# Performance work log

Measured on AMD Instinct MI355X. Metric: run time of the kernel, lower is better.

## Reference

```python
import jax, jax.numpy as jnp
import numpy as np

N_HEAD = 16
LN_EPS = 1e-5


def _layernorm(x, g, b):
    mu = jnp.mean(x, axis=-1, keepdims=True)
    var = jnp.mean(jnp.square(x - mu), axis=-1, keepdims=True)
    return (x - mu) * jax.lax.rsqrt(var + LN_EPS) * g + b


def setup_inputs() -> dict:
    key = jax.random.key(0)
    ks = jax.random.split(key, 12)
    B, S, D = 2, 2048, 1024
    F = 4 * D
    std = 0.02
    return {
        "x": jax.random.normal(ks[0], (B, S, D), jnp.float32),
        "w_attn": jax.random.normal(ks[1], (D, 3 * D), jnp.float32) * std,
        "b_attn": jnp.zeros((3 * D,), jnp.float32),
        "w_o": jax.random.normal(ks[2], (D, D), jnp.float32) * std,
        "b_o": jnp.zeros((D,), jnp.float32),
        "ln1_g": jnp.ones((D,), jnp.float32),
        "ln1_b": jnp.zeros((D,), jnp.float32),
        "w_fc": jax.random.normal(ks[3], (D, F), jnp.float32) * std,
        "b_fc": jnp.zeros((F,), jnp.float32),
        "w_pr": jax.random.normal(ks[4], (F, D), jnp.float32) * std,
        "b_pr": jnp.zeros((D,), jnp.float32),
        "ln2_g": jnp.ones((D,), jnp.float32),
        "ln2_b": jnp.zeros((D,), jnp.float32),
    }


def reference(x, w_attn, b_attn, w_o, b_o, ln1_g, ln1_b,
              w_fc, b_fc, w_pr, b_pr, ln2_g, ln2_b):
    B, S, D = x.shape
    H = N_HEAD
    hd = D // H

    # --- attention ---
    qkv = x @ w_attn + b_attn                      # [B,S,3D]
    q, k, v = jnp.split(qkv, 3, axis=-1)
    q = q.reshape(B, S, H, hd).transpose(0, 2, 1, 3)  # [B,H,S,hd]
    k = k.reshape(B, S, H, hd).transpose(0, 2, 1, 3)
    v = v.reshape(B, S, H, hd).transpose(0, 2, 1, 3)

    # scores in fp32, scaled by sqrt(head_dim) (scale=True)
    w = jnp.einsum('bhqd,bhkd->bhqk', q.astype(jnp.float32),
                   k.astype(jnp.float32)) / jnp.sqrt(jnp.float32(hd))
    bias = jnp.tril(jnp.ones((S, S), jnp.float32))     # causal mask slice of registered buffer
    w = w * bias + (-10000.0) * (1.0 - bias)
    a = jax.nn.softmax(w, axis=-1).astype(v.dtype)
    o = jnp.einsum('bhqk,bhkd->bhqd', a, v)            # [B,H,S,hd]
    o = o.transpose(0, 2, 1, 3).reshape(B, S, D)
    a_out = o @ w_o + b_o

    # --- post-LN residual + MLP (gelu, d_ff = 4D) ---
    n = _layernorm(x + a_out, ln1_g, ln1_b)
    m = jax.nn.gelu(n @ w_fc + b_fc, approximate=False) @ w_pr + b_pr
    h = _layernorm(n + m, ln2_g, ln2_b)
    return h
```

## Files before the change

### kernel.cpp

```cpp
#include <hip/hip_runtime.h>
#include <stdint.h>
#include <math.h>


typedef __attribute__((ext_vector_type(4))) float f32x4;
typedef __attribute__((ext_vector_type(8))) short s16x8;

__device__ __forceinline__ float bf2f(short s){
  unsigned u = ((unsigned)(unsigned short)s) << 16;
  return __builtin_bit_cast(float, u);
}
__device__ __forceinline__ short f2bf(float f){
  unsigned u = __builtin_bit_cast(unsigned, f);
  unsigned r = (u + 0x7fffu + ((u >> 16) & 1u)) >> 16;
  return (short)(unsigned short)r;
}

__device__ __forceinline__ void gload_lds16(const void* gp, void* lp){
  __builtin_amdgcn_global_load_lds(
      (__attribute__((address_space(1))) void*)const_cast<void*>(gp),
      (__attribute__((address_space(3))) void*)lp,
      16, 0, 0);
}

__global__ void cvt_f32_bf16(const float* __restrict__ in, short* __restrict__ out, int n){
  int i = (blockIdx.x * blockDim.x + threadIdx.x) * 4;
  if (i < n){
    float4 v = *(const float4*)(in + i);
    short4 o;
    o.x = f2bf(v.x); o.y = f2bf(v.y); o.z = f2bf(v.z); o.w = f2bf(v.w);
    *(short4*)(out + i) = o;
  }
}

__global__ __launch_bounds__(256) void wtrans(const float* __restrict__ in,
                                              short* __restrict__ out, int R, int C){
  __shared__ float tile[32][33];
  int c0 = blockIdx.x * 32, r0 = blockIdx.y * 32;
  int tx = threadIdx.x, ty = threadIdx.y;
  #pragma unroll
  for (int j = 0; j < 4; ++j)
    tile[ty + j*8][tx] = in[(size_t)(r0 + ty + j*8) * C + c0 + tx];
  __syncthreads();
  #pragma unroll
  for (int j = 0; j < 4; ++j)
    out[(size_t)(c0 + ty + j*8) * R + r0 + tx] = f2bf(tile[tx][ty + j*8]);
}

__global__ __launch_bounds__(256) void vtrans(const short* __restrict__ qkv,
                                              short* __restrict__ vt){
  __shared__ short tile[32][33];
  int bh = blockIdx.z; int b = bh >> 4, h = bh & 15;
  int s0 = blockIdx.x * 32, d0 = blockIdx.y * 32;
  int tx = threadIdx.x, ty = threadIdx.y;
  #pragma unroll
  for (int j = 0; j < 4; ++j)
    tile[ty + j*8][tx] = qkv[(size_t)(b*2048 + s0 + ty + j*8) * 3072 + 2048 + h*64 + d0 + tx];
  __syncthreads();
  #pragma unroll
  for (int j = 0; j < 4; ++j)
    vt[(size_t)(bh*64 + d0 + ty + j*8) * 2048 + s0 + tx] = tile[tx][ty + j*8];
}

#define TBK 32

__global__ __launch_bounds__(512, 2) void gemm256(
    const short* __restrict__ A, const short* __restrict__ BT,
    const float* __restrict__ bias,
    void* __restrict__ o0, void* __restrict__ o1,
    void* __restrict__ o2, void* __restrict__ o3,
    int M, int N, int K, int EPI, int KS)
{
  __shared__ __attribute__((aligned(16))) short lds[4][16384];
  const int t = threadIdx.x;
  const int lane = t & 63;
  const int wid = t >> 6;
  const int wr = wid >> 2, wc = wid & 3;
  const int lrow = lane & 15, lk = lane >> 4;

  const int gx = gridDim.x;
  const int nwg = gx * gridDim.y;
  const int P = blockIdx.y * gx + blockIdx.x;
  const int wg = (P & 7) * (nwg >> 3) + (P >> 3);
  const int m0 = (wg / gx) * 256, n0 = (wg % gx) * 256;

  const int Kspl = K / KS;
  const int kbeg = blockIdx.z * Kspl;
  const int NT = Kspl / TBK;

  const short* srcA[2]; const short* srcB[2]; int ldso[2];
  #pragma unroll
  for (int q = 0; q < 2; ++q){
    int o = q*8192 + t*16;
    int row = o >> 6;
    int chunk = ((o >> 4) & 3) ^ ((row >> 1) & 3);
    ldso[q] = o;
    srcA[q] = A  + (size_t)(m0 + row) * K + kbeg + chunk * 8;
    srcB[q] = BT + (size_t)(n0 + row) * K + kbeg + chunk * 8;
  }

  int aoff[8], boff[4];
  #pragma unroll
  for (int m = 0; m < 8; ++m){
    int row = wr*128 + m*16 + lrow;
    aoff[m] = row*32 + (lk ^ ((row >> 1) & 3))*8;
  }
  #pragma unroll
  for (int n = 0; n < 4; ++n){
    int row = wc*64 + n*16 + lrow;
    boff[n] = 8192 + row*32 + (lk ^ ((row >> 1) & 3))*8;
  }

  auto stage = [&](int tile){
    const int s = tile & 3;
    const int ko = tile * TBK;
    #pragma unroll
    for (int q = 0; q < 2; ++q){
      gload_lds16(srcA[q] + ko, (char*)&lds[s][0] + ldso[q]);
      gload_lds16(srcB[q] + ko, (char*)&lds[s][0] + 16384 + ldso[q]);
    }
  };

  f32x4 acc[8][4] = {};

  stage(0);
  stage(1);
  for (int tt = 0; tt < NT; ++tt){
    if (tt < NT - 1) asm volatile("s_waitcnt vmcnt(4)" ::: "memory");
    else             asm volatile("s_waitcnt vmcnt(0)" ::: "memory");
    __builtin_amdgcn_s_barrier();
    __builtin_amdgcn_sched_barrier(0);

    if (tt + 2 < NT) stage(tt + 2);

    const short* lp = &lds[tt & 3][0];
    s16x8 afr[8], bfr[4];
    #pragma unroll
    for (int n = 0; n < 4; ++n) bfr[n] = *(const s16x8*)(lp + boff[n]);
    #pragma unroll
    for (int m = 0; m < 8; ++m) afr[m] = *(const s16x8*)(lp + aoff[m]);

    asm volatile("s_waitcnt lgkmcnt(0)" ::: "memory");
    __builtin_amdgcn_sched_barrier(0);
    __builtin_amdgcn_s_setprio(1);
    #pragma unroll
    for (int m = 0; m < 8; ++m)
      #pragma unroll
      for (int n = 0; n < 4; ++n)
        acc[m][n] = __builtin_amdgcn_mfma_f32_16x16x32_bf16(afr[m], bfr[n], acc[m][n], 0, 0, 0);
    __builtin_amdgcn_s_setprio(0);
  }

  void* pz = (blockIdx.z == 0) ? o0 : (blockIdx.z == 1) ? o1
           : (blockIdx.z == 2) ? o2 : o3;
  #pragma unroll
  for (int m = 0; m < 8; ++m){
    #pragma unroll
    for (int n = 0; n < 4; ++n){
      #pragma unroll
      for (int r = 0; r < 4; ++r){
        int row = m0 + wr*128 + m*16 + lk*4 + r;
        int col = n0 + wc*64  + n*16 + lrow;
        size_t idx = (size_t)row * N + col;
        if (EPI == 4){
          ((short*)pz)[idx] = f2bf(acc[m][n][r]);
        } else {
          float v = acc[m][n][r] + bias[col];
          if (EPI == 0){
            ((short*)o0)[idx] = f2bf(v);
          } else {
            float g = 0.5f * v * (1.0f + erff(v * 0.70710678118654752f));
            ((short*)o0)[idx] = f2bf(g);
          }
        }
      }
    }
  }
}

__global__ __launch_bounds__(256, 2) void attn_kernel(
    const short* __restrict__ qkv, const short* __restrict__ vt,
    short* __restrict__ ob)
{
  const int P = blockIdx.x;
  const int xcd = P & 7;
  const int idx = P >> 3;
  const int pairi = idx & 15;
  const int bh = xcd + ((idx >> 4) << 3);
  const int b = bh >> 4, h = bh & 15;
  const int t  = threadIdx.x;
  const int lane = t & 63;
  const int w = t >> 6;
  const int lrow = lane & 15, lk = lane >> 4;

  __shared__ short sK[2][64*64];
  __shared__ short sV[2][64*64];
  __shared__ short sP[4][16][68];

  const size_t kgbase = (size_t)(b*2048)*3072 + 1024 + h*64;
  const size_t vgbase = (size_t)((b*16 + h)*64)*2048;

  auto stage = [&](int buf, int k0){
    #pragma unroll
    for (int r2 = 0; r2 < 2; ++r2){
      int o = r2*4096 + t*16;
      int row = o >> 7;
      int lsl = ((o >> 4) & 7) ^ (row & 7);
      gload_lds16(qkv + kgbase + (size_t)(k0 + row)*3072 + lsl*8, (char*)sK[buf] + o);
      gload_lds16(vt  + vgbase + (size_t)row*2048 + k0   + lsl*8, (char*)sV[buf] + o);
    }
  };

  for (int pass = 0; pass < 2; ++pass){
    const int qt = pass ? 31 - pairi : pairi;
    const int q0 = qt * 64;
    const int qbase = q0 + w * 16;

    s16x8 aq[2];
    #pragma unroll
    for (int kc = 0; kc < 2; ++kc)
      aq[kc] = *(const s16x8*)(qkv + (size_t)(b*2048 + qbase + lrow)*3072 + h*64 + kc*32 + lk*8);

    f32x4 oacc[4] = {};
    float mrun[4], lrun[4];
    #pragma unroll
    for (int r = 0; r < 4; ++r){ mrun[r] = -1e30f; lrun[r] = 0.0f; }

    const int nt = qt + 1;
    __syncthreads();
    stage(0, 0);
    __syncthreads();
    int cur = 0;

    for (int ktile = 0; ktile < nt; ++ktile){
      const int k0 = ktile * 64;
      if (ktile + 1 < nt) stage(cur ^ 1, k0 + 64);

      f32x4 sacc[4] = {};
      __builtin_amdgcn_s_setprio(1);
      #pragma unroll
      for (int kc = 0; kc < 2; ++kc){
        #pragma unroll
        for (int ct = 0; ct < 4; ++ct){
          int row = ct*16 + lrow;
          int slot = (kc*4 + lk) ^ (row & 7);
          s16x8 bk = *(const s16x8*)&sK[cur][row*64 + slot*8];
          sacc[ct] = __builtin_amdgcn_mfma_f32_16x16x32_bf16(aq[kc], bk, sacc[ct], 0, 0, 0);
        }
      }
      __builtin_amdgcn_s_setprio(0);

      float s[4][4];
      const bool need_mask = (k0 + 63 > qbase);
      #pragma unroll
      for (int ct = 0; ct < 4; ++ct){
        #pragma unroll
        for (int r = 0; r < 4; ++r){
          float v = sacc[ct][r] * 0.125f;
          if (need_mask){
            int qi = qbase + lk*4 + r;
            int ki = k0 + ct*16 + lrow;
            if (ki > qi) v = -10000.0f;
          }
          s[ct][r] = v;
        }
      }

      #pragma unroll
      for (int r = 0; r < 4; ++r){
        float mx = fmaxf(fmaxf(s[0][r], s[1][r]), fmaxf(s[2][r], s[3][r]));
        #pragma unroll
        for (int off = 1; off < 16; off <<= 1)
          mx = fmaxf(mx, __shfl_xor(mx, off, 64));
        float mnew = fmaxf(mrun[r], mx);
        float sf = __expf(mrun[r] - mnew);
        lrun[r] *= sf;
        #pragma unroll
        for (int dt = 0; dt < 4; ++dt) oacc[dt][r] *= sf;
        float ts = 0.0f;
        #pragma unroll
        for (int ct = 0; ct < 4; ++ct){
          float p = __expf(s[ct][r] - mnew);
          s[ct][r] = p;
          ts += p;
        }
        #pragma unroll
        for (int off = 1; off < 16; off <<= 1)
          ts += __shfl_xor(ts, off, 64);
        lrun[r] += ts;
        mrun[r] = mnew;
      }

      #pragma unroll
      for (int ct = 0; ct < 4; ++ct)
        #pragma unroll
        for (int r = 0; r < 4; ++r)
          sP[w][lk*4 + r][ct*16 + lrow] = f2bf(s[ct][r]);

      s16x8 pa[2];
      #pragma unroll
      for (int kc = 0; kc < 2; ++kc)
        pa[kc] = *(const s16x8*)&sP[w][lrow][kc*32 + lk*8];
      __builtin_amdgcn_s_setprio(1);
      #pragma unroll
      for (int dt = 0; dt < 4; ++dt){
        #pragma unroll
        for (int kc = 0; kc < 2; ++kc){
          int row = dt*16 + lrow;
          int slot = (kc*4 + lk) ^ (row & 7);
          s16x8 bv = *(const s16x8*)&sV[cur][row*64 + slot*8];
          oacc[dt] = __builtin_amdgcn_mfma_f32_16x16x32_bf16(pa[kc], bv, oacc[dt], 0, 0, 0);
        }
      }
      __builtin_amdgcn_s_setprio(0);

      __syncthreads();
      cur ^= 1;
    }

    #pragma unroll
    for (int r = 0; r < 4; ++r){
      float inv = 1.0f / lrun[r];
      int row = b*2048 + qbase + lk*4 + r;
      #pragma unroll
      for (int dt = 0; dt < 4; ++dt){
        int col = h*64 + dt*16 + lrow;
        ob[(size_t)row * 1024 + col] = f2bf(oacc[dt][r] * inv);
      }
    }
  }
}

__global__ __launch_bounds__(256) void ln_fused(
    const short* __restrict__ p0, const short* __restrict__ p1,
    const short* __restrict__ p2, const short* __restrict__ p3,
    const float* __restrict__ bias,
    const short* __restrict__ resid_bf, const float* __restrict__ resid_f,
    const float* __restrict__ g, const float* __restrict__ b,
    void* __restrict__ out, int bf16_out)
{
  const int row = blockIdx.x;
  const int t = threadIdx.x;
  const size_t base = (size_t)row*1024 + t*4;
  short4 a0 = *(const short4*)(p0 + base);
  short4 a1 = *(const short4*)(p1 + base);
  short4 a2 = *(const short4*)(p2 + base);
  short4 a3 = *(const short4*)(p3 + base);
  float4 bi = *(const float4*)(bias + t*4);
  float r0, r1, r2, r3;
  if (resid_bf){
    short4 rr = *(const short4*)(resid_bf + base);
    r0 = bf2f(rr.x); r1 = bf2f(rr.y); r2 = bf2f(rr.z); r3 = bf2f(rr.w);
  } else {
    float4 rr = *(const float4*)(resid_f + base);
    r0 = rr.x; r1 = rr.y; r2 = rr.z; r3 = rr.w;
  }
  float v0 = bf2f(a0.x) + bf2f(a1.x) + bf2f(a2.x) + bf2f(a3.x) + bi.x + r0;
  float v1 = bf2f(a0.y) + bf2f(a1.y) + bf2f(a2.y) + bf2f(a3.y) + bi.y + r1;
  float v2 = bf2f(a0.z) + bf2f(a1.z) + bf2f(a2.z) + bf2f(a3.z) + bi.z + r2;
  float v3 = bf2f(a0.w) + bf2f(a1.w) + bf2f(a2.w) + bf2f(a3.w) + bi.w + r3;
  float s = v0 + v1 + v2 + v3;
  float q = v0*v0 + v1*v1 + v2*v2 + v3*v3;
  #pragma unroll
  for (int off = 1; off < 64; off <<= 1){
    s += __shfl_xor(s, off, 64);
    q += __shfl_xor(q, off, 64);
  }
  __shared__ float ss[4], sq[4];
  if ((t & 63) == 0){ ss[t >> 6] = s; sq[t >> 6] = q; }
  __syncthreads();
  s = ss[0] + ss[1] + ss[2] + ss[3];
  q = sq[0] + sq[1] + sq[2] + sq[3];
  float mu = s * (1.0f/1024.0f);
  float var = q * (1.0f/1024.0f) - mu*mu;
  float rs = rsqrtf(var + 1e-5f);
  float4 gg = *(const float4*)(g + t*4);
  float4 bb = *(const float4*)(b + t*4);
  float o0 = (v0 - mu)*rs*gg.x + bb.x;
  float o1 = (v1 - mu)*rs*gg.y + bb.y;
  float o2 = (v2 - mu)*rs*gg.z + bb.z;
  float o3 = (v3 - mu)*rs*gg.w + bb.w;
  if (bf16_out){
    short4 o; o.x = f2bf(o0); o.y = f2bf(o1); o.z = f2bf(o2); o.w = f2bf(o3);
    *(short4*)((short*)out + base) = o;
  } else {
    float4 o = {o0, o1, o2, o3};
    *(float4*)((float*)out + base) = o;
  }
}

extern "C" void kernel_launch(void* const* d_in, const int* in_sizes, int n_in,
                              void* d_out, int out_size, void* d_ws, size_t ws_size,
                              hipStream_t stream) {
  const float* x      = (const float*)d_in[0];
  const float* w_attn = (const float*)d_in[1];
  const float* b_attn = (const float*)d_in[2];
  const float* w_o    = (const float*)d_in[3];
  const float* b_o    = (const float*)d_in[4];
  const float* ln1_g  = (const float*)d_in[5];
  const float* ln1_b  = (const float*)d_in[6];
  const float* w_fc   = (const float*)d_in[7];
  const float* b_fc   = (const float*)d_in[8];
  const float* w_pr   = (const float*)d_in[9];
  const float* b_pr   = (const float*)d_in[10];
  const float* ln2_g  = (const float*)d_in[11];
  const float* ln2_b  = (const float*)d_in[12];

  char* ws = (char*)d_ws;
  const size_t MB = 1048576;
  short* waT  = (short*)(ws + 0);
  short* wfT  = (short*)(ws + 6*MB);
  short* wpT  = (short*)(ws + 14*MB);
  short* woT  = (short*)(ws + 22*MB);
  short* xb   = (short*)(ws + 24*MB);
  short* vt   = (short*)(ws + 24*MB);
  short* pp2  = (short*)(ws + 24*MB);
  short* qkvb = (short*)(ws + 32*MB);
  short* fb   = (short*)(ws + 32*MB);
  short* ob   = (short*)(ws + 56*MB);
  short* pp0  = (short*)(ws + 64*MB);
  short* pp1  = (short*)(ws + 72*MB);
  short* nb   = (short*)(ws + 80*MB);
  short* pp3  = (short*)(ws + 88*MB);

  const int M = 4096;

  cvt_f32_bf16<<<dim3(M*1024/1024), dim3(256), 0, stream>>>(x, xb, M*1024);
  wtrans<<<dim3(3072/32, 1024/32), dim3(32,8), 0, stream>>>(w_attn, waT, 1024, 3072);
  wtrans<<<dim3(1024/32, 1024/32), dim3(32,8), 0, stream>>>(w_o,   woT, 1024, 1024);
  wtrans<<<dim3(4096/32, 1024/32), dim3(32,8), 0, stream>>>(w_fc,  wfT, 1024, 4096);
  wtrans<<<dim3(1024/32, 4096/32), dim3(32,8), 0, stream>>>(w_pr,  wpT, 4096, 1024);
  gemm256<<<dim3(3072/256, M/256, 1), dim3(512), 0, stream>>>(
      xb, waT, b_attn, qkvb, nullptr, nullptr, nullptr, M, 3072, 1024, 0, 1);
  vtrans<<<dim3(2048/32, 64/32, 32), dim3(32,8), 0, stream>>>(qkvb, vt);
  attn_kernel<<<dim3(512), dim3(256), 0, stream>>>(qkvb, vt, ob);
  gemm256<<<dim3(1024/256, M/256, 4), dim3(512), 0, stream>>>(
      ob, woT, nullptr, pp0, pp1, pp2, pp3, M, 1024, 1024, 4, 4);
  ln_fused<<<dim3(M), dim3(256), 0, stream>>>(pp0, pp1, pp2, pp3, b_o,
                                              nullptr, x, ln1_g, ln1_b, nb, 1);
  gemm256<<<dim3(4096/256, M/256, 1), dim3(512), 0, stream>>>(
      nb, wfT, b_fc, fb, nullptr, nullptr, nullptr, M, 4096, 1024, 2, 1);
  gemm256<<<dim3(1024/256, M/256, 4), dim3(512), 0, stream>>>(
      fb, wpT, nullptr, pp0, pp1, pp2, pp3, M, 1024, 4096, 4, 4);
  ln_fused<<<dim3(M), dim3(256), 0, stream>>>(pp0, pp1, pp2, pp3, b_pr,
                                              nb, nullptr, ln2_g, ln2_b, d_out, 0);
}
```

Measured before the change: 297.5 us.

## Switch GEMM to BK=64 double-buffered LDS pipeline with 8-way swizzle

Reworks the 256x256 GEMM main loop from a 4-stage ring of 32-wide K tiles to two 64-wide K buffers. Each iteration prefetches the next tile, runs two 32-wide MFMA sub-steps, then waits and barriers once. The row length doubles to 128 bytes, so the XOR swizzle moves to 8 chunks. This halves the number of barriers per K, at the cost of shallower prefetch and a full vmcnt(0) wait at the end of every iteration, which could expose load latency.

```diff
diff --git a/kernel.cpp b/kernel.cpp
--- a/kernel.cpp
+++ b/kernel.cpp
@@ -62,8 +62,6 @@
     vt[(size_t)(bh*64 + d0 + ty + j*8) * 2048 + s0 + tx] = tile[tx][ty + j*8];
 }
 
-#define TBK 32
-
 __global__ __launch_bounds__(512, 2) void gemm256(
     const short* __restrict__ A, const short* __restrict__ BT,
     const float* __restrict__ bias,
@@ -71,7 +69,7 @@
     void* __restrict__ o2, void* __restrict__ o3,
     int M, int N, int K, int EPI, int KS)
 {
-  __shared__ __attribute__((aligned(16))) short lds[4][16384];
+  __shared__ __attribute__((aligned(16))) short lds[2][32768];
   const int t = threadIdx.x;
   const int lane = t & 63;
   const int wid = t >> 6;
@@ -86,69 +84,74 @@
 
   const int Kspl = K / KS;
   const int kbeg = blockIdx.z * Kspl;
-  const int NT = Kspl / TBK;
-
-  const short* srcA[2]; const short* srcB[2]; int ldso[2];
-  #pragma unroll
-  for (int q = 0; q < 2; ++q){
-    int o = q*8192 + t*16;
-    int row = o >> 6;
-    int chunk = ((o >> 4) & 3) ^ ((row >> 1) & 3);
-    ldso[q] = o;
-    srcA[q] = A  + (size_t)(m0 + row) * K + kbeg + chunk * 8;
-    srcB[q] = BT + (size_t)(n0 + row) * K + kbeg + chunk * 8;
-  }
-
-  int aoff[8], boff[4];
-  #pragma unroll
-  for (int m = 0; m < 8; ++m){
-    int row = wr*128 + m*16 + lrow;
-    aoff[m] = row*32 + (lk ^ ((row >> 1) & 3))*8;
-  }
-  #pragma unroll
-  for (int n = 0; n < 4; ++n){
-    int row = wc*64 + n*16 + lrow;
-    boff[n] = 8192 + row*32 + (lk ^ ((row >> 1) & 3))*8;
-  }
-
-  auto stage = [&](int tile){
-    const int s = tile & 3;
-    const int ko = tile * TBK;
-    #pragma unroll
-    for (int q = 0; q < 2; ++q){
-      gload_lds16(srcA[q] + ko, (char*)&lds[s][0] + ldso[q]);
-      gload_lds16(srcB[q] + ko, (char*)&lds[s][0] + 16384 + ldso[q]);
+  const int NT = Kspl / 64;
+
+  const short* gsrcA[4]; const short* gsrcB[4]; int ldso[4];
+  #pragma unroll
+  for (int r = 0; r < 4; ++r){
+    int o = r*8192 + t*16;
+    int row = o >> 7;
+    int lsl = ((o >> 4) & 7) ^ (row & 7);
+    ldso[r] = o;
+    gsrcA[r] = A  + (size_t)(m0 + row) * K + kbeg + lsl*8;
+    gsrcB[r] = BT + (size_t)(n0 + row) * K + kbeg + lsl*8;
+  }
+
+  int aoff[2][8], boff[2][4];
+  #pragma unroll
+  for (int kc = 0; kc < 2; ++kc){
+    #pragma unroll
+    for (int m = 0; m < 8; ++m){
+      int row = wr*128 + m*16 + lrow;
+      aoff[kc][m] = row*64 + ((kc*4 + lk) ^ (row & 7))*8;
+    }
+    #pragma unroll
+    for (int n = 0; n < 4; ++n){
+      int row = wc*64 + n*16 + lrow;
+      boff[kc][n] = 16384 + row*64 + ((kc*4 + lk) ^ (row & 7))*8;
+    }
+  }
+
+  auto stage = [&](int buf, int tt){
+    const int ko = tt * 64;
+    char* base = (char*)&lds[buf][0];
+    #pragma unroll
+    for (int r = 0; r < 4; ++r){
+      gload_lds16(gsrcA[r] + ko, base + ldso[r]);
+      gload_lds16(gsrcB[r] + ko, base + 32768 + ldso[r]);
     }
   };
 
   f32x4 acc[8][4] = {};
 
-  stage(0);
-  stage(1);
+  stage(0, 0);
+  asm volatile("s_waitcnt vmcnt(0)" ::: "memory");
+  __builtin_amdgcn_s_barrier();
+  int cur = 0;
+
   for (int tt = 0; tt < NT; ++tt){
-    if (tt < NT - 1) asm volatile("s_waitcnt vmcnt(4)" ::: "memory");
-    else             asm volatile("s_waitcnt vmcnt(0)" ::: "memory");
+    if (tt + 1 < NT) stage(cur ^ 1, tt + 1);
+    const short* lp = &lds[cur][0];
+    #pragma unroll
+    for (int kc = 0; kc < 2; ++kc){
+      s16x8 afr[8], bfr[4];
+      #pragma unroll
+      for (int n = 0; n < 4; ++n) bfr[n] = *(const s16x8*)(lp + boff[kc][n]);
+      #pragma unroll
+      for (int m = 0; m < 8; ++m) afr[m] = *(const s16x8*)(lp + aoff[kc][m]);
+      asm volatile("s_waitcnt lgkmcnt(0)" ::: "memory");
+      __builtin_amdgcn_sched_barrier(0);
+      __builtin_amdgcn_s_setprio(1);
+      #pragma unroll
+      for (int m = 0; m < 8; ++m)
+        #pragma unroll
+        for (int n = 0; n < 4; ++n)
+          acc[m][n] = __builtin_amdgcn_mfma_f32_16x16x32_bf16(afr[m], bfr[n], acc[m][n], 0, 0, 0);
+      __builtin_amdgcn_s_setprio(0);
+    }
+    asm volatile("s_waitcnt vmcnt(0)" ::: "memory");
     __builtin_amdgcn_s_barrier();
-    __builtin_amdgcn_sched_barrier(0);
-
-    if (tt + 2 < NT) stage(tt + 2);
-
-    const short* lp = &lds[tt & 3][0];
-    s16x8 afr[8], bfr[4];
-    #pragma unroll
-    for (int n = 0; n < 4; ++n) bfr[n] = *(const s16x8*)(lp + boff[n]);
-    #pragma unroll
-    for (int m = 0; m < 8; ++m) afr[m] = *(const s16x8*)(lp + aoff[m]);
-
-    asm volatile("s_waitcnt lgkmcnt(0)" ::: "memory");
-    __builtin_amdgcn_sched_barrier(0);
-    __builtin_amdgcn_s_setprio(1);
-    #pragma unroll
-    for (int m = 0; m < 8; ++m)
-      #pragma unroll
-      for (int n = 0; n < 4; ++n)
-        acc[m][n] = __builtin_amdgcn_mfma_f32_16x16x32_bf16(afr[m], bfr[n], acc[m][n], 0, 0, 0);
-    __builtin_amdgcn_s_setprio(0);
+    cur ^= 1;
   }
 
   void* pz = (blockIdx.z == 0) ? o0 : (blockIdx.z == 1) ? o1
```

Result: no change. 297.7 us (+0.1%).
